# Performance work log

Measured on AMD Instinct MI355X. Metric: run time of the kernel, lower is better.

## Reference

```python
import jax, jax.numpy as jnp
import numpy as np

NUM_RECORDS = 10000
NUM_CODES = 128
CODE_DIM = 128
BATCH = 32
NUM_POINTS = 4096
EPS = 1e-16


def setup_inputs() -> dict:
    key = jax.random.key(0)
    k1, k2, k3, k4 = jax.random.split(key, 4)
    indices = jax.random.randint(k1, (BATCH,), 0, NUM_RECORDS)
    query_points = jax.random.uniform(k2, (BATCH, NUM_POINTS, 3), dtype=jnp.float32) - 0.5
    codes_position = jax.random.uniform(k3, (NUM_RECORDS, NUM_CODES, 3), dtype=jnp.float32) - 0.5
    codes = jax.random.normal(k4, (NUM_RECORDS, NUM_CODES, CODE_DIM), dtype=jnp.float32) * 0.01
    return {
        "indices": indices,
        "query_points": query_points,
        "codes_position": codes_position,
        "codes": codes,
        "dist_scale": 2,
    }


def reference(indices, query_points, codes_position, codes, dist_scale):
    # Gather per-record code clouds: (B, C, 3) and (B, C, D)
    batch_pos = codes_position[indices]
    batch_codes = codes[indices]
    # Pairwise squared distance: (B, P, C)
    diff = query_points[:, :, None, :] - batch_pos[:, None, :, :]
    square_dist = jnp.sum(diff * diff, axis=-1) + EPS
    # Inverse-distance weights: 1 / sqrt(d)^s, normalized over codes
    weight = 1.0 / jnp.sqrt(square_dist) ** dist_scale
    weight = weight / jnp.sum(weight, axis=-1, keepdims=True)
    # Weighted sum of codes: (B, P, C) @ (B, C, D) -> (B, P, D)
    query_codes = jnp.einsum('bpc,bcd->bpd', weight, batch_codes)
    return (query_codes, square_dist, weight)
```

## Files before the change

kernel.cpp:

```cpp
#include <hip/hip_runtime.h>
#include <hip/hip_bf16.h>

#define NB 32
#define NP 4096
#define NC 128
#define ND 128
#define TP 64
#define EPSV 1e-16f

typedef __attribute__((ext_vector_type(8))) short short8;
typedef __attribute__((ext_vector_type(4))) short short4v;
typedef __attribute__((ext_vector_type(4))) float f32x4;

__device__ __forceinline__ unsigned short f2bf(float f) {
  __hip_bfloat16 h = __float2bfloat16(f);
  return *reinterpret_cast<unsigned short*>(&h);
}

__device__ __forceinline__ int swz(int row, int kbyte) {
  return (row * 256 + kbyte) ^ ((row & 7) << 4);
}

__global__ void cc_pre(const int* __restrict__ indices,
                       const float* __restrict__ codes,
                       unsigned char* __restrict__ ws) {
  const int b = blockIdx.x >> 3;
  const int chunk = blockIdx.x & 7;
  const int rec = indices[b];
  const float* cb = codes + (size_t)rec * (NC * ND);
  unsigned char* wb = ws + (size_t)b * (NC * ND * 2);
  const int tid = threadIdx.x;
  const int d = chunk * 16 + (tid & 15);
  const int c0 = (tid >> 4) * 8;
  short8 v;
  #pragma unroll
  for (int j = 0; j < 8; ++j)
    v[j] = (short)f2bf(cb[(size_t)(c0 + j) * ND + d]);
  *(short8*)(wb + swz(d, c0 * 2)) = v;
}

template<bool PRE>
__global__ __launch_bounds__(256, 2) void cc_main(
    const int* __restrict__ indices,
    const float* __restrict__ qp,
    const float* __restrict__ cpos,
    const float* __restrict__ codes,
    const void* __restrict__ dsp,
    const unsigned char* __restrict__ wsc,
    float* __restrict__ out_qc,
    float* __restrict__ out_sq,
    float* __restrict__ out_wt) {
  __shared__ __align__(16) unsigned char cT[ND * NC * 2];
  __shared__ __align__(16) unsigned char wT[TP * NC * 2];

  const int tid = threadIdx.x;
  const int lane = tid & 63;
  const int wv = tid >> 6;
  const int g = lane >> 4;
  const int l16 = lane & 15;
  const int b = blockIdx.x >> 6;
  const int p0 = (blockIdx.x & 63) * TP;
  const int rec = indices[b];
  unsigned char* wTw = wT + wv * (16 * 256);

  const int si = ((const int*)dsp)[0];
  const float sv = (si > 0 && si < 1000) ? (float)si : ((const float*)dsp)[0];

  if (PRE) {
    const unsigned char* src = wsc + (size_t)b * (NC * ND * 2);
    #pragma unroll
    for (int it = 0; it < 8; ++it) {
      const int off = (wv * 8 + it) * 1024;
      __builtin_amdgcn_global_load_lds(
          (const __attribute__((address_space(1))) void*)(src + off + lane * 16),
          (__attribute__((address_space(3))) void*)(cT + off),
          16, 0, 0);
    }
  } else {
    const float* cb = codes + (size_t)rec * (NC * ND);
    #pragma unroll
    for (int it = 0; it < 16; ++it) {
      int i = tid * 4 + it * 1024;
      float4 v = *reinterpret_cast<const float4*>(cb + i);
      int c = i >> 7, d0 = i & 127;
      float vv[4] = {v.x, v.y, v.z, v.w};
      #pragma unroll
      for (int j = 0; j < 4; ++j)
        *(unsigned short*)(cT + swz(d0 + j, c * 2)) = f2bf(vv[j]);
    }
  }

  const float* pb0 = cpos + ((size_t)rec * NC + l16 * 4) * 3;
  const float* pb1 = cpos + ((size_t)rec * NC + 64 + l16 * 4) * 3;
  float px[8], py[8], pz[8];
  #pragma unroll
  for (int j = 0; j < 4; ++j) {
    px[j] = pb0[j * 3 + 0]; py[j] = pb0[j * 3 + 1]; pz[j] = pb0[j * 3 + 2];
    px[j + 4] = pb1[j * 3 + 0]; py[j + 4] = pb1[j * 3 + 1]; pz[j + 4] = pb1[j * 3 + 2];
  }

  const size_t rowbase = (size_t)b * NP + p0;
  float qx[4], qy[4], qz[4];
  #pragma unroll
  for (int it = 0; it < 4; ++it) {
    const int p = wv * 16 + it * 4 + g;
    const float* q = qp + (rowbase + p) * 3;
    qx[it] = q[0]; qy[it] = q[1]; qz[it] = q[2];
  }

  __syncthreads();

  const bool s2 = (sv == 2.0f);
  #pragma unroll
  for (int it = 0; it < 4; ++it) {
    const int p = wv * 16 + it * 4 + g;
    float dd[8], wu[8];
    #pragma unroll
    for (int j = 0; j < 8; ++j) {
      const float dx = qx[it] - px[j], dy = qy[it] - py[j], dz = qz[it] - pz[j];
      dd[j] = fmaf(dx, dx, fmaf(dy, dy, dz * dz)) + EPSV;
    }
    if (s2) {
      #pragma unroll
      for (int j = 0; j < 8; ++j) wu[j] = __builtin_amdgcn_rcpf(dd[j]);
    } else {
      #pragma unroll
      for (int j = 0; j < 8; ++j) wu[j] = __powf(dd[j], -0.5f * sv);
    }
    float s = ((wu[0] + wu[1]) + (wu[2] + wu[3])) + ((wu[4] + wu[5]) + (wu[6] + wu[7]));
    s += __shfl_xor(s, 1); s += __shfl_xor(s, 2);
    s += __shfl_xor(s, 4); s += __shfl_xor(s, 8);
    const float inv = __builtin_amdgcn_rcpf(s);

    f32x4 dlo, dhi, wlo, whi;
    #pragma unroll
    for (int j = 0; j < 4; ++j) {
      dlo[j] = dd[j]; dhi[j] = dd[j + 4];
      wlo[j] = wu[j] * inv; whi[j] = wu[j + 4] * inv;
    }
    const size_t rb = (rowbase + p) * (size_t)NC;
    *(f32x4*)(out_sq + rb + l16 * 4) = dlo;
    *(f32x4*)(out_sq + rb + 64 + l16 * 4) = dhi;
    *(f32x4*)(out_wt + rb + l16 * 4) = wlo;
    *(f32x4*)(out_wt + rb + 64 + l16 * 4) = whi;

    short4v wbl, wbh;
    #pragma unroll
    for (int j = 0; j < 4; ++j) {
      wbl[j] = (short)f2bf(wlo[j]);
      wbh[j] = (short)f2bf(whi[j]);
    }
    const int r = it * 4 + g;
    *(short4v*)(wTw + swz(r, l16 * 8)) = wbl;
    *(short4v*)(wTw + swz(r, 128 + l16 * 8)) = wbh;
  }


  const int kg = lane >> 4;
  const int prl = wv * 16 + l16;
  f32x4 acc[8];
  #pragma unroll
  for (int mi = 0; mi < 8; ++mi) acc[mi] = (f32x4){0.f, 0.f, 0.f, 0.f};

  #pragma unroll
  for (int kk = 0; kk < NC; kk += 32) {
    const int kb = (kk + kg * 8) * 2;
    const short8 b0 = *(const short8*)(wTw + swz(l16, kb));
    #pragma unroll
    for (int mi = 0; mi < 8; ++mi) {
      const short8 a8 = *(const short8*)(cT + swz(mi * 16 + l16, kb));
      acc[mi] = __builtin_amdgcn_mfma_f32_16x16x32_bf16(a8, b0, acc[mi], 0, 0, 0);
    }
  }

  float* o0 = out_qc + (rowbase + prl) * (size_t)ND + kg * 4;
  #pragma unroll
  for (int mi = 0; mi < 8; ++mi)
    *(f32x4*)(o0 + mi * 16) = acc[mi];

  (void)codes;
}

extern "C" void kernel_launch(void* const* d_in, const int* in_sizes, int n_in,
                              void* d_out, int out_size, void* d_ws, size_t ws_size,
                              hipStream_t stream) {
  const int* indices = (const int*)d_in[0];
  const float* qp = (const float*)d_in[1];
  const float* cpos = (const float*)d_in[2];
  const float* codes = (const float*)d_in[3];
  const void* dsp = d_in[4];

  float* out = (float*)d_out;
  float* qc = out;
  float* sq = qc + (size_t)NB * NP * ND;
  float* wt = sq + (size_t)NB * NP * NC;

  const size_t ws_need = (size_t)NB * NC * ND * 2;
  dim3 grid(NB * (NP / TP));
  if (ws_size >= ws_need) {
    cc_pre<<<dim3(NB * 8), dim3(256), 0, stream>>>(indices, codes, (unsigned char*)d_ws);
    cc_main<true><<<grid, 256, 0, stream>>>(indices, qp, cpos, codes, dsp,
                                            (const unsigned char*)d_ws, qc, sq, wt);
  } else {
    cc_main<false><<<grid, 256, 0, stream>>>(indices, qp, cpos, codes, dsp,
                                             nullptr, qc, sq, wt);
  }
}
```

Before: 43.21 us.

## Load code MFMA fragments directly from global into registers, drop LDS staging

The pre-pass now writes the bf16 codes in MFMA fragment order, so each lane can load its A-operand fragments with contiguous 16-byte global loads. The main kernel no longer stages the 32KB code tile in shared memory and drops the block-wide barrier. Fragments are double-buffered in registers and loaded one k-step ahead of the MFMAs. This cuts LDS usage and may raise occupancy, but adds register pressure and repeats the L2 reads of each batch's codes in every block.

```diff
diff --git a/kernel.cpp b/kernel.cpp
--- a/kernel.cpp
+++ b/kernel.cpp
@@ -29,14 +29,19 @@
   const int rec = indices[b];
   const float* cb = codes + (size_t)rec * (NC * ND);
   unsigned char* wb = ws + (size_t)b * (NC * ND * 2);
-  const int tid = threadIdx.x;
-  const int d = chunk * 16 + (tid & 15);
-  const int c0 = (tid >> 4) * 8;
+  const int id = chunk * 256 + threadIdx.x;
+  const int lane = id & 63;
+  const int l16 = lane & 15;
+  const int kg = (lane >> 4) & 3;
+  const int mi = (id >> 6) & 7;
+  const int kk = id >> 9;
+  const int d = mi * 16 + l16;
+  const int cbase = kk * 32 + kg * 8;
   short8 v;
   #pragma unroll
   for (int j = 0; j < 8; ++j)
-    v[j] = (short)f2bf(cb[(size_t)(c0 + j) * ND + d]);
-  *(short8*)(wb + swz(d, c0 * 2)) = v;
+    v[j] = (short)f2bf(cb[(size_t)(cbase + j) * ND + d]);
+  *(short8*)(wb + ((size_t)id * 16)) = v;
 }
 
 template<bool PRE>
@@ -50,7 +55,6 @@
     float* __restrict__ out_qc,
     float* __restrict__ out_sq,
     float* __restrict__ out_wt) {
-  __shared__ __align__(16) unsigned char cT[ND * NC * 2];
   __shared__ __align__(16) unsigned char wT[TP * NC * 2];
 
   const int tid = threadIdx.x;
@@ -66,30 +70,6 @@
   const int si = ((const int*)dsp)[0];
   const float sv = (si > 0 && si < 1000) ? (float)si : ((const float*)dsp)[0];
 
-  if (PRE) {
-    const unsigned char* src = wsc + (size_t)b * (NC * ND * 2);
-    #pragma unroll
-    for (int it = 0; it < 8; ++it) {
-      const int off = (wv * 8 + it) * 1024;
-      __builtin_amdgcn_global_load_lds(
-          (const __attribute__((address_space(1))) void*)(src + off + lane * 16),
-          (__attribute__((address_space(3))) void*)(cT + off),
-          16, 0, 0);
-    }
-  } else {
-    const float* cb = codes + (size_t)rec * (NC * ND);
-    #pragma unroll
-    for (int it = 0; it < 16; ++it) {
-      int i = tid * 4 + it * 1024;
-      float4 v = *reinterpret_cast<const float4*>(cb + i);
-      int c = i >> 7, d0 = i & 127;
-      float vv[4] = {v.x, v.y, v.z, v.w};
-      #pragma unroll
-      for (int j = 0; j < 4; ++j)
-        *(unsigned short*)(cT + swz(d0 + j, c * 2)) = f2bf(vv[j]);
-    }
-  }
-
   const float* pb0 = cpos + ((size_t)rec * NC + l16 * 4) * 3;
   const float* pb1 = cpos + ((size_t)rec * NC + 64 + l16 * 4) * 3;
   float px[8], py[8], pz[8];
@@ -108,7 +88,21 @@
     qx[it] = q[0]; qy[it] = q[1]; qz[it] = q[2];
   }
 
-  __syncthreads();
+  const unsigned char* fb = wsc + (size_t)b * (NC * ND * 2) + (size_t)lane * 16;
+  const float* cb = codes + (size_t)rec * (NC * ND);
+  short8 fA[8], fB[8];
+  #pragma unroll
+  for (int mi = 0; mi < 8; ++mi) {
+    if (PRE) {
+      fA[mi] = *(const short8*)(fb + (0 * 8 + mi) * 1024);
+    } else {
+      const int d = mi * 16 + l16;
+      const int cbase0 = g * 8;
+      #pragma unroll
+      for (int j = 0; j < 8; ++j)
+        fA[mi][j] = (short)f2bf(cb[(size_t)(cbase0 + j) * ND + d]);
+    }
+  }
 
   const bool s2 = (sv == 2.0f);
   #pragma unroll
@@ -155,30 +149,51 @@
     *(short4v*)(wTw + swz(r, 128 + l16 * 8)) = wbh;
   }
 
-
   const int kg = lane >> 4;
   const int prl = wv * 16 + l16;
   f32x4 acc[8];
   #pragma unroll
   for (int mi = 0; mi < 8; ++mi) acc[mi] = (f32x4){0.f, 0.f, 0.f, 0.f};
 
-  #pragma unroll
-  for (int kk = 0; kk < NC; kk += 32) {
-    const int kb = (kk + kg * 8) * 2;
-    const short8 b0 = *(const short8*)(wTw + swz(l16, kb));
-    #pragma unroll
-    for (int mi = 0; mi < 8; ++mi) {
-      const short8 a8 = *(const short8*)(cT + swz(mi * 16 + l16, kb));
-      acc[mi] = __builtin_amdgcn_mfma_f32_16x16x32_bf16(a8, b0, acc[mi], 0, 0, 0);
-    }
-  }
+  #define LOADF(dst, kknext)                                                   \
+    _Pragma("unroll")                                                          \
+    for (int mi = 0; mi < 8; ++mi) {                                           \
+      if (PRE) {                                                               \
+        dst[mi] = *(const short8*)(fb + ((kknext) * 8 + mi) * 1024);           \
+      } else {                                                                 \
+        const int d = mi * 16 + l16;                                           \
+        const int cb0 = (kknext) * 32 + g * 8;                                 \
+        _Pragma("unroll")                                                      \
+        for (int j = 0; j < 8; ++j)                                            \
+          dst[mi][j] = (short)f2bf(cb[(size_t)(cb0 + j) * ND + d]);            \
+      }                                                                        \
+    }
+
+  #define COMPUTE(src, kk)                                                     \
+    {                                                                          \
+      const int kb = ((kk) * 32 + kg * 8) * 2;                                 \
+      const short8 b0 = *(const short8*)(wTw + swz(l16, kb));                  \
+      _Pragma("unroll")                                                        \
+      for (int mi = 0; mi < 8; ++mi)                                           \
+        acc[mi] = __builtin_amdgcn_mfma_f32_16x16x32_bf16(src[mi], b0,         \
+                                                          acc[mi], 0, 0, 0);   \
+    }
+
+  LOADF(fB, 1)
+  COMPUTE(fA, 0)
+  LOADF(fA, 2)
+  COMPUTE(fB, 1)
+  LOADF(fB, 3)
+  COMPUTE(fA, 2)
+  COMPUTE(fB, 3)
+
+  #undef LOADF
+  #undef COMPUTE
 
   float* o0 = out_qc + (rowbase + prl) * (size_t)ND + kg * 4;
   #pragma unroll
   for (int mi = 0; mi < 8; ++mi)
     *(f32x4*)(o0 + mi * 16) = acc[mi];
-
-  (void)codes;
 }
 
 extern "C" void kernel_launch(void* const* d_in, const int* in_sizes, int n_in,
```

Result: no change. 42.40 us (-1.9%).
